# Kernel optimization log

Hardware: AMD Instinct MI355X
Metric: run time of the kernel (lower is better)

Reference implementation:

```python
import jax, jax.numpy as jnp
import numpy as np

H = 1024
NH = 16
HD = H // NH
EPS = 1e-5

def setup_inputs() -> dict:
    key = jax.random.key(0)
    ks = jax.random.split(key, 5)
    B, S = 2, 2048
    scale = 1.0 / np.sqrt(H)
    return {
        "x": jax.random.normal(ks[0], (B, S, H), dtype=jnp.float32),
        "Wq": jax.random.normal(ks[1], (H, H), dtype=jnp.float32) * scale,
        "Wk": jax.random.normal(ks[2], (H, H), dtype=jnp.float32) * scale,
        "Wv": jax.random.normal(ks[3], (H, H), dtype=jnp.float32) * scale,
        "Wo": jax.random.normal(ks[4], (H, H), dtype=jnp.float32) * scale,
        "bo": jnp.zeros((H,), dtype=jnp.float32),
        "gamma": jnp.ones((H,), dtype=jnp.float32),
        "beta": jnp.zeros((H,), dtype=jnp.float32),
    }

def reference(x, Wq, Wk, Wv, Wo, bo, gamma, beta):
    B, S, _ = x.shape
    residual = x
    # pre-LayerNorm
    mu = jnp.mean(x, axis=-1, keepdims=True)
    var = jnp.mean(jnp.square(x - mu), axis=-1, keepdims=True)
    xn = (x - mu) * jax.lax.rsqrt(var + EPS) * gamma + beta
    # QKV projections (torch Linear: y = x @ W.T), split heads -> [B, NH, S, HD]
    q = (xn @ Wq.T).reshape(B, S, NH, HD).transpose(0, 2, 1, 3)
    k = (xn @ Wk.T).reshape(B, S, NH, HD).transpose(0, 2, 1, 3)
    v = (xn @ Wv.T).reshape(B, S, NH, HD).transpose(0, 2, 1, 3)
    # naive attention: explicit [B, NH, S, S] scores
    scale = 1.0 / np.sqrt(HD)
    scores = jnp.einsum('bhqd,bhkd->bhqk', q, k) * scale
    attn = jax.nn.softmax(scores.astype(jnp.float32), axis=-1).astype(q.dtype)
    out = jnp.einsum('bhqk,bhkd->bhqd', attn, v)
    out = out.transpose(0, 2, 1, 3).reshape(B, S, H)
    out = out @ Wo.T + bo
    return out + residual
```

## Files before the change

kernel.cpp:

```cpp
#include <hip/hip_runtime.h>
#include <hip/hip_bf16.h>

#define H 1024
#define NHEAD 16
#define HDIM 64
#define SEQ 2048
#define BATCH 2
#define M_TOT (BATCH * SEQ)
#define NQKV 3072

typedef __attribute__((ext_vector_type(8))) short bf16x8;
typedef __attribute__((ext_vector_type(4))) float f32x4;

#define C2_SCALE 0.18033688f

__device__ __forceinline__ unsigned short f2bf(float f) {
  union { float f; unsigned int u; } a;
  a.f = f;
  unsigned int u = a.u;
  return (unsigned short)((u + 0x7fffu + ((u >> 16) & 1u)) >> 16);
}

__device__ __forceinline__ unsigned int pkbf(float a, float b) {
  union { __hip_bfloat162 h; unsigned int u; } cv;
  cv.h = __float22bfloat162_rn(float2{a, b});
  return cv.u;
}

__device__ __forceinline__ float fast_exp2(float x) {
#if defined(__has_builtin) && __has_builtin(__builtin_amdgcn_exp2f)
  return __builtin_amdgcn_exp2f(x);
#else
  return exp2f(x);
#endif
}

typedef const __attribute__((address_space(1))) void* gas1_t;
typedef __attribute__((address_space(3))) void* las3_t;
__device__ __forceinline__ void gload16(const void* g, void* l) {
  __builtin_amdgcn_global_load_lds((gas1_t)(unsigned long long)g,
                                   (las3_t)(unsigned int)(unsigned long long)l,
                                   16, 0, 0);
}

__global__ __launch_bounds__(256) void ln_cast_kernel(const float* __restrict__ x,
                                                      const float* __restrict__ gamma,
                                                      const float* __restrict__ beta,
                                                      unsigned short* __restrict__ xn,
                                                      const float* __restrict__ w0,
                                                      const float* __restrict__ w1,
                                                      const float* __restrict__ w2,
                                                      const float* __restrict__ w3,
                                                      unsigned short* __restrict__ wdst) {
  const int t = threadIdx.x;
  if (blockIdx.x >= M_TOT) {
    const int cb = blockIdx.x - M_TOT;
    const int y = cb >> 10;
    const float* s = (y == 0) ? w0 : (y == 1) ? w1 : (y == 2) ? w2 : w3;
    const int i = (cb & 1023) * 256 + t;
    const float4 v = ((const float4*)s)[i];
    ushort4 o;
    o.x = f2bf(v.x);
    o.y = f2bf(v.y);
    o.z = f2bf(v.z);
    o.w = f2bf(v.w);
    ((ushort4*)(wdst + (size_t)y * H * H))[i] = o;
    return;
  }
  const int row = blockIdx.x;
  const float* xr = x + (size_t)row * H;
  float4 v = ((const float4*)xr)[t];
  float s = v.x + v.y + v.z + v.w;
  float s2 = v.x * v.x + v.y * v.y + v.z * v.z + v.w * v.w;
#pragma unroll
  for (int o = 32; o; o >>= 1) {
    s += __shfl_xor(s, o, 64);
    s2 += __shfl_xor(s2, o, 64);
  }
  __shared__ float red[8];
  const int wave = t >> 6;
  if ((t & 63) == 0) {
    red[wave] = s;
    red[wave + 4] = s2;
  }
  __syncthreads();
  const float ts = red[0] + red[1] + red[2] + red[3];
  const float ts2 = red[4] + red[5] + red[6] + red[7];
  const float mu = ts * (1.0f / (float)H);
  const float var = ts2 * (1.0f / (float)H) - mu * mu;
  const float rstd = rsqrtf(var + 1e-5f);
  const float4 g = ((const float4*)gamma)[t];
  const float4 b = ((const float4*)beta)[t];
  ushort4 o;
  o.x = f2bf((v.x - mu) * rstd * g.x + b.x);
  o.y = f2bf((v.y - mu) * rstd * g.y + b.y);
  o.z = f2bf((v.z - mu) * rstd * g.z + b.z);
  o.w = f2bf((v.w - mu) * rstd * g.w + b.w);
  ((ushort4*)(xn + (size_t)row * H))[t] = o;
}

template <int EPI, int NPX>
__global__ __launch_bounds__(256, 4) void gemm128(const unsigned short* __restrict__ A,
                                                  const unsigned short* __restrict__ W,
                                                  unsigned short* __restrict__ qk,
                                                  unsigned short* __restrict__ vt,
                                                  const float* __restrict__ bo,
                                                  const float* __restrict__ x,
                                                  float* __restrict__ out) {
  const int id = blockIdx.x;
  const int xcd = id & 7;
  const int r = id >> 3;
  const int nb = xcd * NPX + (r % NPX);
  const int mb = r / NPX;
  const int m0 = mb * 128;
  const int n0 = nb * 128;
  const int tid = threadIdx.x;
  const int wave = tid >> 6;
  const int lane = tid & 63;
  const int l16 = lane & 15;
  const int quad = lane >> 4;
  const int wx = wave & 1, wy = wave >> 1;

  __shared__ __align__(16) unsigned short As[2][128 * 32];
  __shared__ __align__(16) unsigned short Bs[2][128 * 32];

  const int sub = lane >> 2;
  const int kcol = (lane & 3) * 8;
  const unsigned short* ag = A + (size_t)(m0 + wave * 32 + sub) * H + kcol;
  const unsigned short* bg = W + (size_t)(n0 + wave * 32 + sub) * H + kcol;
  const int lofs = wave * 32 * 32;

  f32x4 acc[4][4] = {};

  gload16(ag, &As[0][lofs]);
  gload16(ag + 16 * H, &As[0][lofs + 16 * 32]);
  gload16(bg, &Bs[0][lofs]);
  gload16(bg + 16 * H, &Bs[0][lofs + 16 * 32]);

  for (int it = 0; it < H / 32; it++) {
    const int bi = it & 1;
    __syncthreads();
    if (it + 1 < H / 32) {
      const int k1 = (it + 1) * 32;
      gload16(ag + k1, &As[bi ^ 1][lofs]);
      gload16(ag + k1 + 16 * H, &As[bi ^ 1][lofs + 16 * 32]);
      gload16(bg + k1, &Bs[bi ^ 1][lofs]);
      gload16(bg + k1 + 16 * H, &Bs[bi ^ 1][lofs + 16 * 32]);
    }
    bf16x8 af[4], bf[4];
#pragma unroll
    for (int t = 0; t < 4; t++) {
      af[t] = *(const bf16x8*)&As[bi][(wy * 64 + t * 16 + l16) * 32 + quad * 8];
      bf[t] = *(const bf16x8*)&Bs[bi][(wx * 64 + t * 16 + l16) * 32 + quad * 8];
    }
#pragma unroll
    for (int i = 0; i < 4; i++)
#pragma unroll
      for (int j = 0; j < 4; j++)
        acc[i][j] = __builtin_amdgcn_mfma_f32_16x16x32_bf16(af[i], bf[j], acc[i][j], 0, 0, 0);
  }

  if (EPI == 0) {
#pragma unroll
    for (int j = 0; j < 4; j++) {
      const int cb = n0 + wx * 64 + j * 16;
      if (cb < 2048) {
        const float qs = (cb < 1024) ? C2_SCALE : 1.0f;
#pragma unroll
        for (int i = 0; i < 4; i++) {
          const int row = m0 + wy * 64 + i * 16 + quad * 4;
#pragma unroll
          for (int r2 = 0; r2 < 4; r2++)
            qk[(size_t)(row + r2) * 2048 + cb + l16] = f2bf(acc[i][j][r2] * qs);
        }
      } else {
        const int n = cb + l16 - 2048;
#pragma unroll
        for (int i = 0; i < 4; i++) {
          const int row0 = m0 + wy * 64 + i * 16 + quad * 4;
          const int b = row0 >> 11;
          const int s = row0 & 2047;
          ushort4 p;
          p.x = f2bf(acc[i][j][0]);
          p.y = f2bf(acc[i][j][1]);
          p.z = f2bf(acc[i][j][2]);
          p.w = f2bf(acc[i][j][3]);
          *(ushort4*)&vt[((size_t)b * 1024 + n) * SEQ + s] = p;
        }
      }
    }
  } else {
#pragma unroll
    for (int j = 0; j < 4; j++) {
      const int col = n0 + wx * 64 + j * 16 + l16;
      const float bv = bo[col];
#pragma unroll
      for (int i = 0; i < 4; i++) {
        const int row = m0 + wy * 64 + i * 16 + quad * 4;
#pragma unroll
        for (int r2 = 0; r2 < 4; r2++) {
          const size_t idx = (size_t)(row + r2) * H + col;
          out[idx] = acc[i][j][r2] + bv + x[idx];
        }
      }
    }
  }
}

__global__ __launch_bounds__(256, 2) void attn_kernel(const unsigned short* __restrict__ qk,
                                                      const unsigned short* __restrict__ vt,
                                                      unsigned short* __restrict__ O) {
  const int id = blockIdx.x;
  const int xcd = id & 7;
  const int slot = id >> 3;
  const int qt = slot & 15;
  const int g = slot >> 4;
  const int combo = xcd * 4 + g;
  const int h = combo & 15;
  const int b = combo >> 4;
  const int tid = threadIdx.x;
  const int wave = tid >> 6;
  const int lane = tid & 63;
  const int l16 = lane & 15;
  const int quad = lane >> 4;
  const int l8 = l16 & 7;

  __shared__ __align__(16) unsigned short Kt[2][64 * 64];
  __shared__ __align__(16) unsigned short Vt[2][64 * 64];
  __shared__ __align__(16) unsigned short Pt[8][16 * 64];

  const unsigned short* Qbase = qk + (size_t)b * SEQ * 2048 + h * 64;
  const unsigned short* Kbase = qk + (size_t)b * SEQ * 2048 + 1024 + h * 64;
  const unsigned short* Vbase = vt + ((size_t)b * 1024 + h * 64) * SEQ;

  const int rIn = lane >> 3;
  const int gsw = (lane & 7) ^ rIn;
  const int ch0 = 2 * wave;

  const int qrow0 = qt * 128 + wave * 32 + l16;
  bf16x8 aq[2][2];
#pragma unroll
  for (int u = 0; u < 2; u++)
#pragma unroll
    for (int c = 0; c < 2; c++)
      aq[u][c] = *(const bf16x8*)(Qbase + (size_t)(qrow0 + u * 16) * 2048 + c * 32 + quad * 8);

  float lacc[2][2] = {};
  f32x4 o_acc[2][4] = {};

#pragma unroll
  for (int c = 0; c < 2; c++) {
    const int ch = ch0 + c;
    const int row = ch * 8 + rIn;
    gload16(Kbase + (size_t)row * 2048 + gsw * 8, &Kt[0][ch * 512]);
    gload16(Vbase + (size_t)row * SEQ + gsw * 8, &Vt[0][ch * 512]);
  }

  unsigned short* myP0 = &Pt[wave * 2 + 0][0];
  unsigned short* myP1 = &Pt[wave * 2 + 1][0];

#pragma unroll 2
  for (int it = 0; it < SEQ / 64; it++) {
    const int bi = it & 1;
    __syncthreads();
    if (it + 1 < SEQ / 64) {
#pragma unroll
      for (int c = 0; c < 2; c++) {
        const int ch = ch0 + c;
        const int row = ch * 8 + rIn;
        gload16(Kbase + (size_t)((it + 1) * 64 + row) * 2048 + gsw * 8,
                &Kt[bi ^ 1][ch * 512]);
        gload16(Vbase + (size_t)row * SEQ + (it + 1) * 64 + gsw * 8,
                &Vt[bi ^ 1][ch * 512]);
      }
    }

    f32x4 s[2][4] = {};
#pragma unroll
    for (int c = 0; c < 2; c++) {
#pragma unroll
      for (int t = 0; t < 4; t++) {
        const bf16x8 kf =
            *(const bf16x8*)&Kt[bi][(t * 16 + l16) * 64 + (((c * 4 + quad) ^ l8) * 8)];
        s[0][t] = __builtin_amdgcn_mfma_f32_16x16x32_bf16(kf, aq[0][c], s[0][t], 0, 0, 0);
        s[1][t] = __builtin_amdgcn_mfma_f32_16x16x32_bf16(kf, aq[1][c], s[1][t], 0, 0, 0);
      }
    }

    float pv[2][4][4];
#pragma unroll
    for (int u = 0; u < 2; u++)
#pragma unroll
      for (int t = 0; t < 4; t++) {
#pragma unroll
        for (int r = 0; r < 4; r++) pv[u][t][r] = fast_exp2(s[u][t][r]);
        lacc[u][t & 1] += (pv[u][t][0] + pv[u][t][1]) + (pv[u][t][2] + pv[u][t][3]);
      }

#pragma unroll
    for (int t = 0; t < 4; t++) {
      const int wofs = l16 * 64 + (((t * 2 + (quad >> 1)) ^ l8) * 8) + (quad & 1) * 4;
      uint2 d0, d1;
      d0.x = pkbf(pv[0][t][0], pv[0][t][1]);
      d0.y = pkbf(pv[0][t][2], pv[0][t][3]);
      d1.x = pkbf(pv[1][t][0], pv[1][t][1]);
      d1.y = pkbf(pv[1][t][2], pv[1][t][3]);
      *(uint2*)&myP0[wofs] = d0;
      *(uint2*)&myP1[wofs] = d1;
    }

#pragma unroll
    for (int c = 0; c < 2; c++) {
      const int rofs = l16 * 64 + (((c * 4 + quad) ^ l8) * 8);
      const bf16x8 pb0 = *(const bf16x8*)&myP0[rofs];
      const bf16x8 pb1 = *(const bf16x8*)&myP1[rofs];
#pragma unroll
      for (int dt = 0; dt < 4; dt++) {
        const bf16x8 vf =
            *(const bf16x8*)&Vt[bi][(dt * 16 + l16) * 64 + (((c * 4 + quad) ^ l8) * 8)];
        o_acc[0][dt] = __builtin_amdgcn_mfma_f32_16x16x32_bf16(vf, pb0, o_acc[0][dt], 0, 0, 0);
        o_acc[1][dt] = __builtin_amdgcn_mfma_f32_16x16x32_bf16(vf, pb1, o_acc[1][dt], 0, 0, 0);
      }
    }
  }

#pragma unroll
  for (int u = 0; u < 2; u++) {
    float l_i = lacc[u][0] + lacc[u][1];
    l_i += __shfl_xor(l_i, 16, 64);
    l_i += __shfl_xor(l_i, 32, 64);
    const float inv = 1.0f / l_i;
    unsigned short* orow = O + ((size_t)(b * SEQ + qrow0 + u * 16)) * H + h * 64;
#pragma unroll
    for (int dt = 0; dt < 4; dt++) {
      uint2 d;
      d.x = pkbf(o_acc[u][dt][0] * inv, o_acc[u][dt][1] * inv);
      d.y = pkbf(o_acc[u][dt][2] * inv, o_acc[u][dt][3] * inv);
      *(uint2*)&orow[dt * 16 + quad * 4] = d;
    }
  }
}

extern "C" void kernel_launch(void* const* d_in, const int* in_sizes, int n_in,
                              void* d_out, int out_size, void* d_ws, size_t ws_size,
                              hipStream_t stream) {
  const float* x = (const float*)d_in[0];
  const float* Wq = (const float*)d_in[1];
  const float* Wk = (const float*)d_in[2];
  const float* Wv = (const float*)d_in[3];
  const float* Wo = (const float*)d_in[4];
  const float* bo = (const float*)d_in[5];
  const float* gamma = (const float*)d_in[6];
  const float* beta = (const float*)d_in[7];
  float* out = (float*)d_out;

  unsigned short* ws = (unsigned short*)d_ws;
  unsigned short* xn = ws;
  unsigned short* wcat = xn + (size_t)M_TOT * H;
  unsigned short* wob = wcat + (size_t)3 * H * H;
  unsigned short* qkb = wcat + (size_t)4 * H * H;
  unsigned short* vtb = qkb + (size_t)M_TOT * 2048;
  unsigned short* atb = vtb + (size_t)BATCH * H * SEQ;

  ln_cast_kernel<<<M_TOT + 4096, 256, 0, stream>>>(x, gamma, beta, xn, Wq, Wk, Wv, Wo,
                                                   wcat);
  gemm128<0, 3><<<(M_TOT / 128) * (NQKV / 128), 256, 0, stream>>>(
      xn, wcat, qkb, vtb, nullptr, nullptr, nullptr);
  attn_kernel<<<(SEQ / 128) * NHEAD * BATCH, 256, 0, stream>>>(qkb, vtb, atb);
  gemm128<1, 1><<<(M_TOT / 128) * (H / 128), 256, 0, stream>>>(
      atb, wob, nullptr, nullptr, bo, x, out);
}
```

Before: 194.5 us.

## Switch attention to 32x32x16 MFMA and pass P via permlane32 swap

Rewrites the attention inner loop to use 32x32x16 bf16 MFMA tiles instead of 16x16x32. Each wave now covers 32 query rows with a single accumulator layout. The exp'd score tile is converted to the PV operand layout in registers with permlane32_swap, which removes the per-wave LDS round-trip for P and its shared buffer. This cuts LDS traffic and instruction count, but the larger accumulators raise register pressure and the new lane mapping must be exactly right for correctness.

```diff
diff --git a/kernel.cpp b/kernel.cpp
--- a/kernel.cpp
+++ b/kernel.cpp
@@ -11,6 +11,7 @@
 
 typedef __attribute__((ext_vector_type(8))) short bf16x8;
 typedef __attribute__((ext_vector_type(4))) float f32x4;
+typedef __attribute__((ext_vector_type(16))) float f32x16;
 
 #define C2_SCALE 0.18033688f
 
@@ -221,13 +222,12 @@
   const int tid = threadIdx.x;
   const int wave = tid >> 6;
   const int lane = tid & 63;
-  const int l16 = lane & 15;
-  const int quad = lane >> 4;
-  const int l8 = l16 & 7;
+  const int l31 = lane & 31;
+  const int l7 = lane & 7;
+  const int hi = lane >> 5;
 
   __shared__ __align__(16) unsigned short Kt[2][64 * 64];
   __shared__ __align__(16) unsigned short Vt[2][64 * 64];
-  __shared__ __align__(16) unsigned short Pt[8][16 * 64];
 
   const unsigned short* Qbase = qk + (size_t)b * SEQ * 2048 + h * 64;
   const unsigned short* Kbase = qk + (size_t)b * SEQ * 2048 + 1024 + h * 64;
@@ -237,16 +237,14 @@
   const int gsw = (lane & 7) ^ rIn;
   const int ch0 = 2 * wave;
 
-  const int qrow0 = qt * 128 + wave * 32 + l16;
-  bf16x8 aq[2][2];
-#pragma unroll
-  for (int u = 0; u < 2; u++)
-#pragma unroll
-    for (int c = 0; c < 2; c++)
-      aq[u][c] = *(const bf16x8*)(Qbase + (size_t)(qrow0 + u * 16) * 2048 + c * 32 + quad * 8);
-
-  float lacc[2][2] = {};
-  f32x4 o_acc[2][4] = {};
+  const int qrow = qt * 128 + wave * 32 + l31;
+  bf16x8 aq[4];
+#pragma unroll
+  for (int kc = 0; kc < 4; kc++)
+    aq[kc] = *(const bf16x8*)(Qbase + (size_t)qrow * 2048 + kc * 16 + hi * 8);
+
+  f32x16 o_acc[2] = {};
+  float lc[4] = {};
 
 #pragma unroll
   for (int c = 0; c < 2; c++) {
@@ -255,9 +253,6 @@
     gload16(Kbase + (size_t)row * 2048 + gsw * 8, &Kt[0][ch * 512]);
     gload16(Vbase + (size_t)row * SEQ + gsw * 8, &Vt[0][ch * 512]);
   }
-
-  unsigned short* myP0 = &Pt[wave * 2 + 0][0];
-  unsigned short* myP1 = &Pt[wave * 2 + 1][0];
 
 #pragma unroll 2
   for (int it = 0; it < SEQ / 64; it++) {
@@ -275,70 +270,69 @@
       }
     }
 
-    f32x4 s[2][4] = {};
-#pragma unroll
-    for (int c = 0; c < 2; c++) {
-#pragma unroll
-      for (int t = 0; t < 4; t++) {
-        const bf16x8 kf =
-            *(const bf16x8*)&Kt[bi][(t * 16 + l16) * 64 + (((c * 4 + quad) ^ l8) * 8)];
-        s[0][t] = __builtin_amdgcn_mfma_f32_16x16x32_bf16(kf, aq[0][c], s[0][t], 0, 0, 0);
-        s[1][t] = __builtin_amdgcn_mfma_f32_16x16x32_bf16(kf, aq[1][c], s[1][t], 0, 0, 0);
-      }
-    }
-
-    float pv[2][4][4];
-#pragma unroll
-    for (int u = 0; u < 2; u++)
-#pragma unroll
-      for (int t = 0; t < 4; t++) {
-#pragma unroll
-        for (int r = 0; r < 4; r++) pv[u][t][r] = fast_exp2(s[u][t][r]);
-        lacc[u][t & 1] += (pv[u][t][0] + pv[u][t][1]) + (pv[u][t][2] + pv[u][t][3]);
-      }
-
-#pragma unroll
-    for (int t = 0; t < 4; t++) {
-      const int wofs = l16 * 64 + (((t * 2 + (quad >> 1)) ^ l8) * 8) + (quad & 1) * 4;
-      uint2 d0, d1;
-      d0.x = pkbf(pv[0][t][0], pv[0][t][1]);
-      d0.y = pkbf(pv[0][t][2], pv[0][t][3]);
-      d1.x = pkbf(pv[1][t][0], pv[1][t][1]);
-      d1.y = pkbf(pv[1][t][2], pv[1][t][3]);
-      *(uint2*)&myP0[wofs] = d0;
-      *(uint2*)&myP1[wofs] = d1;
-    }
-
-#pragma unroll
-    for (int c = 0; c < 2; c++) {
-      const int rofs = l16 * 64 + (((c * 4 + quad) ^ l8) * 8);
-      const bf16x8 pb0 = *(const bf16x8*)&myP0[rofs];
-      const bf16x8 pb1 = *(const bf16x8*)&myP1[rofs];
-#pragma unroll
-      for (int dt = 0; dt < 4; dt++) {
-        const bf16x8 vf =
-            *(const bf16x8*)&Vt[bi][(dt * 16 + l16) * 64 + (((c * 4 + quad) ^ l8) * 8)];
-        o_acc[0][dt] = __builtin_amdgcn_mfma_f32_16x16x32_bf16(vf, pb0, o_acc[0][dt], 0, 0, 0);
-        o_acc[1][dt] = __builtin_amdgcn_mfma_f32_16x16x32_bf16(vf, pb1, o_acc[1][dt], 0, 0, 0);
-      }
-    }
-  }
-
-#pragma unroll
-  for (int u = 0; u < 2; u++) {
-    float l_i = lacc[u][0] + lacc[u][1];
-    l_i += __shfl_xor(l_i, 16, 64);
-    l_i += __shfl_xor(l_i, 32, 64);
-    const float inv = 1.0f / l_i;
-    unsigned short* orow = O + ((size_t)(b * SEQ + qrow0 + u * 16)) * H + h * 64;
-#pragma unroll
-    for (int dt = 0; dt < 4; dt++) {
+    f32x16 s_acc[2] = {};
+#pragma unroll
+    for (int kc = 0; kc < 4; kc++) {
+#pragma unroll
+      for (int mt = 0; mt < 2; mt++) {
+        const bf16x8 kf = *(const bf16x8*)&Kt[bi][(mt * 32 + l31) * 64 +
+                                                 ((kc * 16 + hi * 8) ^ (l7 * 8))];
+        s_acc[mt] = __builtin_amdgcn_mfma_f32_32x32x16_bf16(kf, aq[kc], s_acc[mt], 0, 0, 0);
+      }
+    }
+
+    unsigned int w[2][8];
+#pragma unroll
+    for (int mt = 0; mt < 2; mt++) {
+      float p[16];
+#pragma unroll
+      for (int r2 = 0; r2 < 16; r2++) p[r2] = fast_exp2(s_acc[mt][r2]);
+      const float a0 = (p[0] + p[1]) + (p[2] + p[3]);
+      const float a1 = (p[4] + p[5]) + (p[6] + p[7]);
+      const float a2 = (p[8] + p[9]) + (p[10] + p[11]);
+      const float a3 = (p[12] + p[13]) + (p[14] + p[15]);
+      lc[mt * 2 + 0] += a0 + a2;
+      lc[mt * 2 + 1] += a1 + a3;
+#pragma unroll
+      for (int gi = 0; gi < 8; gi++) w[mt][gi] = pkbf(p[2 * gi], p[2 * gi + 1]);
+    }
+
+#pragma unroll
+    for (int sc = 0; sc < 4; sc++) {
+      const int n0i = 2 * sc, n1i = 2 * sc + 1;
+      const int mt0 = n0i >> 2, b0 = n0i & 3;
+      const int mt1 = n1i >> 2, b1 = n1i & 3;
+      const auto rA = __builtin_amdgcn_permlane32_swap(w[mt0][2 * b0], w[mt1][2 * b1],
+                                                       false, false);
+      const auto rB = __builtin_amdgcn_permlane32_swap(w[mt0][2 * b0 + 1], w[mt1][2 * b1 + 1],
+                                                       false, false);
+      union { unsigned int u[4]; bf16x8 v; } pb;
+      pb.u[0] = rA[0];
+      pb.u[1] = rB[0];
+      pb.u[2] = rA[1];
+      pb.u[3] = rB[1];
+#pragma unroll
+      for (int dt = 0; dt < 2; dt++) {
+        const bf16x8 vf = *(const bf16x8*)&Vt[bi][(dt * 32 + l31) * 64 +
+                                                  ((sc * 16 + hi * 8) ^ (l7 * 8))];
+        o_acc[dt] = __builtin_amdgcn_mfma_f32_32x32x16_bf16(vf, pb.v, o_acc[dt], 0, 0, 0);
+      }
+    }
+  }
+
+  float lsum = (lc[0] + lc[1]) + (lc[2] + lc[3]);
+  const float l_i = lsum + __shfl_xor(lsum, 32, 64);
+  const float inv = 1.0f / l_i;
+  unsigned short* orow = O + ((size_t)(b * SEQ + qrow)) * H + h * 64;
+#pragma unroll
+  for (int dt = 0; dt < 2; dt++)
+#pragma unroll
+    for (int rg = 0; rg < 4; rg++) {
       uint2 d;
-      d.x = pkbf(o_acc[u][dt][0] * inv, o_acc[u][dt][1] * inv);
-      d.y = pkbf(o_acc[u][dt][2] * inv, o_acc[u][dt][3] * inv);
-      *(uint2*)&orow[dt * 16 + quad * 4] = d;
-    }
-  }
+      d.x = pkbf(o_acc[dt][4 * rg + 0] * inv, o_acc[dt][4 * rg + 1] * inv);
+      d.y = pkbf(o_acc[dt][4 * rg + 2] * inv, o_acc[dt][4 * rg + 3] * inv);
+      *(uint2*)&orow[dt * 32 + 8 * rg + 4 * hi] = d;
+    }
 }
 
 extern "C" void kernel_launch(void* const* d_in, const int* in_sizes, int n_in,
```

Measured after the change: 191.3 us. Within noise of the previous version (-1.6%).
